# Kernel optimization log

Measured on AMD Instinct MI355X. Metric: run time of the kernel, lower is better.

Reference implementation:

```python
import jax, jax.numpy as jnp
import numpy as np

LAMBDA_TEMP = 20.0
GAMMA = 20.0
MARGIN = 0.05
EPS = 1e-8

B, K, M, D = 128, 256, 8, 128


def _unit(x, axis=-1):
    return x / jnp.linalg.norm(x, axis=axis, keepdims=True)


def setup_inputs() -> dict:
    key = jax.random.key(0)
    k1, k2, k3 = jax.random.split(key, 3)
    v_proj = _unit(jax.random.normal(k1, (B, K, D), dtype=jnp.float32))
    prototypes = _unit(jax.random.normal(k2, (K, M, D), dtype=jnp.float32))
    concept_labels = jax.random.randint(k3, (B, K), 0, 2, dtype=jnp.int64)
    return {"v_proj": v_proj, "concept_labels": concept_labels, "prototypes": prototypes}


def reference(v_proj, concept_labels, prototypes):
    # all-pairs prototype similarities: query vector (b,k) vs prototypes of concept c
    # sims: (B, K, C, M)
    sims = jnp.einsum('bkd,cmd->bkcm', v_proj, prototypes)
    # Eq.6: soft assignment over the M prototypes of each concept
    q = jax.nn.softmax(GAMMA * sims, axis=-1)
    # Eq.7-8: weighted similarity sim_c(v)  -> (B, K, C)
    sim = jnp.sum(q * sims, axis=-1)
    # positive similarity: concept k queried against its own prototypes, plus margin
    sim_pos = jnp.einsum('bkk->bk', sim) + MARGIN  # (B, K)
    # Eq.9: -log( exp(lam*sim_pos) / (sum_c exp(lam*sim_c) + eps) )
    denom = jnp.sum(jnp.exp(LAMBDA_TEMP * sim), axis=-1) + EPS  # (B, K)
    loss_bk = jnp.log(denom) - LAMBDA_TEMP * sim_pos  # (B, K)
    mask = (concept_labels == 1).astype(loss_bk.dtype)
    num_pos = jnp.sum(mask)
    total = jnp.sum(loss_bk * mask)
    return jnp.where(num_pos > 0, total / num_pos, total)
```

## Files before the change

### kernel.cpp

```cpp
#include <hip/hip_runtime.h>

#define NROWS 32768
#define LT 20.0f
#define CHUNKS 32

typedef _Float16 half8 __attribute__((ext_vector_type(8)));
typedef float    f32x4 __attribute__((ext_vector_type(4)));

__device__ __forceinline__ float swz16(float x) {
    return __int_as_float(__builtin_amdgcn_ds_swizzle(__float_as_int(x), 0x401F));
}

__global__ __launch_bounds__(1024)
void mpcl_main(const float* __restrict__ V,
               const int*   __restrict__ labels,
               const float* __restrict__ P,
               int* __restrict__ ws,
               float* __restrict__ out)
{
    __shared__ _Float16 Pst[2][64 * 128];
    __shared__ float sh_denom[128];
    __shared__ float sh_simpos[128];
    __shared__ float sh_red[32];

    int*   gcnt = ws;
    float* gsum = (float*)(ws + 2);

    const int tid  = threadIdx.x;
    const int lane = tid & 63;
    const int w    = tid >> 6;
    const int rg   = w >> 2;
    const int colq = w & 3;
    const int n    = lane & 15;
    const int q    = lane >> 4;
    const int rowbase = blockIdx.x * 128;
    const int cb   = colq * 16;

    if (tid < 128) { sh_denom[tid] = 0.0f; sh_simpos[tid] = 0.0f; }

    half8 vh[2][4];
#pragma unroll
    for (int rf = 0; rf < 2; ++rf) {
        const float* vr = V + (size_t)(rowbase + rg * 32 + rf * 16 + n) * 128 + q * 8;
#pragma unroll
        for (int c = 0; c < 4; ++c) {
            float4 x0 = *(const float4*)(vr + c * 32);
            float4 x1 = *(const float4*)(vr + c * 32 + 4);
            vh[rf][c][0] = (_Float16)x0.x; vh[rf][c][1] = (_Float16)x0.y;
            vh[rf][c][2] = (_Float16)x0.z; vh[rf][c][3] = (_Float16)x0.w;
            vh[rf][c][4] = (_Float16)x1.x; vh[rf][c][5] = (_Float16)x1.y;
            vh[rf][c][6] = (_Float16)x1.z; vh[rf][c][7] = (_Float16)x1.w;
        }
    }

    const int scol = tid >> 4;
    const int sdb  = tid & 15;
    const int sdbs = (sdb & 8) | ((sdb ^ scol) & 7);

    {
        const float* pp = P + (size_t)scol * 128 + sdb * 8;
        float4 a = *(const float4*)(pp);
        float4 b = *(const float4*)(pp + 4);
        half8 hv;
        hv[0] = (_Float16)a.x; hv[1] = (_Float16)a.y;
        hv[2] = (_Float16)a.z; hv[3] = (_Float16)a.w;
        hv[4] = (_Float16)b.x; hv[5] = (_Float16)b.y;
        hv[6] = (_Float16)b.z; hv[7] = (_Float16)b.w;
        *(half8*)&Pst[0][scol * 128 + sdbs * 8] = hv;
    }
    float4 pf0, pf1;
    {
        const float* pp = P + (size_t)(64 + scol) * 128 + sdb * 8;
        pf0 = *(const float4*)(pp);
        pf1 = *(const float4*)(pp + 4);
    }

    float dn[2] = {0.f, 0.f};

#pragma unroll 1
    for (int ch = 0; ch < CHUNKS; ++ch) {
        __syncthreads();

        half8 pf16[4];
#pragma unroll
        for (int c = 0; c < 4; ++c) {
            int dblk = c * 4 + q;
            int col  = cb + n;
            int dbs  = (dblk & 8) | ((dblk ^ col) & 7);
            pf16[c] = *(const half8*)&Pst[ch & 1][col * 128 + dbs * 8];
        }

        f32x4 acc[2] = {{0.f,0.f,0.f,0.f},{0.f,0.f,0.f,0.f}};
#pragma unroll
        for (int c = 0; c < 4; ++c)
#pragma unroll
            for (int rf = 0; rf < 2; ++rf)
                acc[rf] = __builtin_amdgcn_mfma_f32_16x16x32_f16(pf16[c], vh[rf][c], acc[rf], 0, 0, 0);

        if (ch < CHUNKS - 1) {
            half8 hv;
            hv[0] = (_Float16)pf0.x; hv[1] = (_Float16)pf0.y;
            hv[2] = (_Float16)pf0.z; hv[3] = (_Float16)pf0.w;
            hv[4] = (_Float16)pf1.x; hv[5] = (_Float16)pf1.y;
            hv[6] = (_Float16)pf1.z; hv[7] = (_Float16)pf1.w;
            *(half8*)&Pst[(ch + 1) & 1][scol * 128 + sdbs * 8] = hv;
        }
        if (ch < CHUNKS - 2) {
            const float* pp = P + (size_t)((ch + 2) * 64 + scol) * 128 + sdb * 8;
            pf0 = *(const float4*)(pp);
            pf1 = *(const float4*)(pp + 4);
        }

        const int cbase = ch * 8 + colq * 2;
        const int cA    = cbase + (q >> 1);
#pragma unroll
        for (int rf = 0; rf < 2; ++rf) {
            float s0 = acc[rf][0], s1 = acc[rf][1], s2 = acc[rf][2], s3 = acc[rf][3];
            float e0 = __expf(LT * s0), e1 = __expf(LT * s1);
            float e2 = __expf(LT * s2), e3 = __expf(LT * s3);
            float es = (e0 + e1) + (e2 + e3);
            float ss = fmaf(e0, s0, fmaf(e1, s1, fmaf(e2, s2, e3 * s3)));
            es += swz16(es);
            ss += swz16(ss);
            float simc = __fdividef(ss, es);
            dn[rf] += __expf(LT * simc);
            int rowloc = rg * 32 + rf * 16 + n;
            if (cA == ((rowbase + rowloc) & 255) && (q & 1) == 0)
                sh_simpos[rowloc] = simc;
        }
    }

#pragma unroll
    for (int rf = 0; rf < 2; ++rf) {
        float t = dn[rf];
        t += swz16(t);
        t += __shfl_xor(t, 32);
        if (q == 0)
            atomicAdd(&sh_denom[rg * 32 + rf * 16 + n], 0.5f * t);
    }
    __syncthreads();

    float s = 0.f, cc = 0.f;
    if (tid < 128) {
        int row = rowbase + tid;
        float lp = logf(sh_denom[tid] + 1e-8f) - LT * (sh_simpos[tid] + 0.05f);
        float mk = (labels[row] == 1) ? 1.0f : 0.0f;
        s = lp * mk;
        cc = mk;
    }
#pragma unroll
    for (int off = 32; off >= 1; off >>= 1) {
        s  += __shfl_down(s, off);
        cc += __shfl_down(cc, off);
    }
    if (lane == 0) { sh_red[w] = s; sh_red[16 + w] = cc; }
    __syncthreads();
    if (tid == 0) {
        s = 0.f; cc = 0.f;
#pragma unroll
        for (int i = 0; i < 16; ++i) { s += sh_red[i]; cc += sh_red[16 + i]; }
        atomicAdd(&gsum[0], s);
        atomicAdd(&gsum[1], cc);
        __threadfence();
        int g = __hip_atomic_fetch_add(gcnt, 1,
                                       __ATOMIC_ACQ_REL, __HIP_MEMORY_SCOPE_AGENT);
        if (g == 255) {
            __threadfence();
            float ts = __hip_atomic_load(&gsum[0], __ATOMIC_RELAXED, __HIP_MEMORY_SCOPE_AGENT);
            float tc = __hip_atomic_load(&gsum[1], __ATOMIC_RELAXED, __HIP_MEMORY_SCOPE_AGENT);
            out[0] = (tc > 0.0f) ? (ts / tc) : ts;
        }
    }
}

extern "C" void kernel_launch(void* const* d_in, const int* in_sizes, int n_in,
                              void* d_out, int out_size, void* d_ws, size_t ws_size,
                              hipStream_t stream)
{
    const float* V      = (const float*)d_in[0];
    const int*   labels = (const int*)d_in[1];
    const float* P      = (const float*)d_in[2];
    float* out = (float*)d_out;
    int*   ws  = (int*)d_ws;

    hipMemsetAsync(ws, 0, 16, stream);
    mpcl_main<<<256, 1024, 0, stream>>>(V, labels, P, ws, out);
}
```

Before: 115.5 us.

## Pre-convert prototypes to swizzled fp16 and stream via global_load_lds

Adds a prep kernel that converts the prototypes to fp16 once, in a pre-swizzled LDS layout. The main kernel then copies 128-column chunks directly into shared memory with global_load_lds, removing the per-block fp32 load, convert and LDS store work. Each wave now computes two MFMA tiles per chunk so that all 8 prototypes of a concept are held in one lane's registers. This removes the cross-lane swizzle reductions and halves the number of chunk iterations. The cost is an extra kernel launch and a workspace buffer.

```diff
diff --git a/kernel.cpp b/kernel.cpp
--- a/kernel.cpp
+++ b/kernel.cpp
@@ -2,23 +2,48 @@
 
 #define NROWS 32768
 #define LT 20.0f
-#define CHUNKS 32
+#define CHUNKS 16
 
 typedef _Float16 half8 __attribute__((ext_vector_type(8)));
 typedef float    f32x4 __attribute__((ext_vector_type(4)));
 
 __device__ __forceinline__ float swz16(float x) {
     return __int_as_float(__builtin_amdgcn_ds_swizzle(__float_as_int(x), 0x401F));
+}
+
+#define GLD16(gp, lp) __builtin_amdgcn_global_load_lds( \
+    (const __attribute__((address_space(1))) void*)(gp), \
+    (__attribute__((address_space(3))) void*)(lp), 16, 0, 0)
+
+__global__ __launch_bounds__(256)
+void mpcl_prep(const float* __restrict__ P, _Float16* __restrict__ Pw)
+{
+    int id   = blockIdx.x * 256 + threadIdx.x;
+    int gcol = id >> 4;
+    int dblk = id & 15;
+    int ch   = gcol >> 7;
+    int col  = gcol & 127;
+    int key  = (col & 3) | ((col & 8) >> 1);
+    int dbs  = (dblk & 8) | ((dblk ^ key) & 7);
+    const float* src = P + (size_t)gcol * 128 + dblk * 8;
+    float4 a = *(const float4*)src;
+    float4 b = *(const float4*)(src + 4);
+    half8 hv;
+    hv[0] = (_Float16)a.x; hv[1] = (_Float16)a.y;
+    hv[2] = (_Float16)a.z; hv[3] = (_Float16)a.w;
+    hv[4] = (_Float16)b.x; hv[5] = (_Float16)b.y;
+    hv[6] = (_Float16)b.z; hv[7] = (_Float16)b.w;
+    *(half8*)&Pw[((size_t)ch * 2048 + col * 16 + dbs) * 8] = hv;
 }
 
 __global__ __launch_bounds__(1024)
 void mpcl_main(const float* __restrict__ V,
                const int*   __restrict__ labels,
-               const float* __restrict__ P,
+               const _Float16* __restrict__ Pw,
                int* __restrict__ ws,
                float* __restrict__ out)
 {
-    __shared__ _Float16 Pst[2][64 * 128];
+    __shared__ __align__(16) _Float16 Pst[2][2048 * 8];
     __shared__ float sh_denom[128];
     __shared__ float sh_simpos[128];
     __shared__ float sh_red[32];
@@ -34,7 +59,6 @@
     const int n    = lane & 15;
     const int q    = lane >> 4;
     const int rowbase = blockIdx.x * 128;
-    const int cb   = colq * 16;
 
     if (tid < 128) { sh_denom[tid] = 0.0f; sh_simpos[tid] = 0.0f; }
 
@@ -53,27 +77,24 @@
         }
     }
 
-    const int scol = tid >> 4;
-    const int sdb  = tid & 15;
-    const int sdbs = (sdb & 8) | ((sdb ^ scol) & 7);
-
-    {
-        const float* pp = P + (size_t)scol * 128 + sdb * 8;
-        float4 a = *(const float4*)(pp);
-        float4 b = *(const float4*)(pp + 4);
-        half8 hv;
-        hv[0] = (_Float16)a.x; hv[1] = (_Float16)a.y;
-        hv[2] = (_Float16)a.z; hv[3] = (_Float16)a.w;
-        hv[4] = (_Float16)b.x; hv[5] = (_Float16)b.y;
-        hv[6] = (_Float16)b.z; hv[7] = (_Float16)b.w;
-        *(half8*)&Pst[0][scol * 128 + sdbs * 8] = hv;
-    }
-    float4 pf0, pf1;
-    {
-        const float* pp = P + (size_t)(64 + scol) * 128 + sdb * 8;
-        pf0 = *(const float4*)(pp);
-        pf1 = *(const float4*)(pp + 4);
-    }
+    const int col1 = colq * 32 + ((n >> 2) << 3) + (n & 3);
+    int off1[4];
+#pragma unroll
+    for (int c = 0; c < 4; ++c) {
+        int dblk = c * 4 + q;
+        int dbs  = (dblk & 8) | ((dblk ^ (n & 7)) & 7);
+        off1[c]  = (col1 * 16 + dbs) * 8;
+    }
+
+    const _Float16* gbase = Pw + (size_t)(w * 128 + lane) * 8;
+    _Float16* l0 = &Pst[0][(w * 128) * 8];
+    _Float16* l1 = &Pst[1][(w * 128) * 8];
+
+    GLD16(gbase,       l0);
+    GLD16(gbase + 512, l0 + 512);
+
+    const int rowk0 = (rowbase + rg * 32 + n) & 255;
+    const int rowk1 = (rowbase + rg * 32 + 16 + n) & 255;
 
     float dn[2] = {0.f, 0.f};
 
@@ -81,52 +102,43 @@
     for (int ch = 0; ch < CHUNKS; ++ch) {
         __syncthreads();
 
-        half8 pf16[4];
+        if (ch < CHUNKS - 1) {
+            const _Float16* g = gbase + (size_t)(ch + 1) * 16384;
+            _Float16* lnx = (ch & 1) ? l0 : l1;
+            GLD16(g,       lnx);
+            GLD16(g + 512, lnx + 512);
+        }
+
+        const _Float16* base = (ch & 1) ? &Pst[1][0] : &Pst[0][0];
+
+        f32x4 acc1[2] = {{0.f,0.f,0.f,0.f},{0.f,0.f,0.f,0.f}};
+        f32x4 acc2[2] = {{0.f,0.f,0.f,0.f},{0.f,0.f,0.f,0.f}};
 #pragma unroll
         for (int c = 0; c < 4; ++c) {
-            int dblk = c * 4 + q;
-            int col  = cb + n;
-            int dbs  = (dblk & 8) | ((dblk ^ col) & 7);
-            pf16[c] = *(const half8*)&Pst[ch & 1][col * 128 + dbs * 8];
-        }
-
-        f32x4 acc[2] = {{0.f,0.f,0.f,0.f},{0.f,0.f,0.f,0.f}};
-#pragma unroll
-        for (int c = 0; c < 4; ++c)
-#pragma unroll
-            for (int rf = 0; rf < 2; ++rf)
-                acc[rf] = __builtin_amdgcn_mfma_f32_16x16x32_f16(pf16[c], vh[rf][c], acc[rf], 0, 0, 0);
-
-        if (ch < CHUNKS - 1) {
-            half8 hv;
-            hv[0] = (_Float16)pf0.x; hv[1] = (_Float16)pf0.y;
-            hv[2] = (_Float16)pf0.z; hv[3] = (_Float16)pf0.w;
-            hv[4] = (_Float16)pf1.x; hv[5] = (_Float16)pf1.y;
-            hv[6] = (_Float16)pf1.z; hv[7] = (_Float16)pf1.w;
-            *(half8*)&Pst[(ch + 1) & 1][scol * 128 + sdbs * 8] = hv;
-        }
-        if (ch < CHUNKS - 2) {
-            const float* pp = P + (size_t)((ch + 2) * 64 + scol) * 128 + sdb * 8;
-            pf0 = *(const float4*)(pp);
-            pf1 = *(const float4*)(pp + 4);
-        }
-
-        const int cbase = ch * 8 + colq * 2;
-        const int cA    = cbase + (q >> 1);
+            half8 a1 = *(const half8*)&base[off1[c]];
+            half8 a2 = *(const half8*)&base[off1[c] + 512];
+            acc1[0] = __builtin_amdgcn_mfma_f32_16x16x32_f16(a1, vh[0][c], acc1[0], 0, 0, 0);
+            acc1[1] = __builtin_amdgcn_mfma_f32_16x16x32_f16(a1, vh[1][c], acc1[1], 0, 0, 0);
+            acc2[0] = __builtin_amdgcn_mfma_f32_16x16x32_f16(a2, vh[0][c], acc2[0], 0, 0, 0);
+            acc2[1] = __builtin_amdgcn_mfma_f32_16x16x32_f16(a2, vh[1][c], acc2[1], 0, 0, 0);
+        }
+
+        const int cA = ch * 16 + colq * 4 + q;
 #pragma unroll
         for (int rf = 0; rf < 2; ++rf) {
-            float s0 = acc[rf][0], s1 = acc[rf][1], s2 = acc[rf][2], s3 = acc[rf][3];
-            float e0 = __expf(LT * s0), e1 = __expf(LT * s1);
-            float e2 = __expf(LT * s2), e3 = __expf(LT * s3);
-            float es = (e0 + e1) + (e2 + e3);
-            float ss = fmaf(e0, s0, fmaf(e1, s1, fmaf(e2, s2, e3 * s3)));
-            es += swz16(es);
-            ss += swz16(ss);
+            float x0 = acc1[rf][0], x1 = acc1[rf][1], x2 = acc1[rf][2], x3 = acc1[rf][3];
+            float x4 = acc2[rf][0], x5 = acc2[rf][1], x6 = acc2[rf][2], x7 = acc2[rf][3];
+            float e0 = __expf(LT * x0), e1 = __expf(LT * x1);
+            float e2 = __expf(LT * x2), e3 = __expf(LT * x3);
+            float e4 = __expf(LT * x4), e5 = __expf(LT * x5);
+            float e6 = __expf(LT * x6), e7 = __expf(LT * x7);
+            float es = ((e0 + e1) + (e2 + e3)) + ((e4 + e5) + (e6 + e7));
+            float ss = fmaf(e0, x0, fmaf(e1, x1, fmaf(e2, x2, e3 * x3)))
+                     + fmaf(e4, x4, fmaf(e5, x5, fmaf(e6, x6, e7 * x7)));
             float simc = __fdividef(ss, es);
             dn[rf] += __expf(LT * simc);
-            int rowloc = rg * 32 + rf * 16 + n;
-            if (cA == ((rowbase + rowloc) & 255) && (q & 1) == 0)
-                sh_simpos[rowloc] = simc;
+            if (cA == (rf ? rowk1 : rowk0))
+                sh_simpos[rg * 32 + rf * 16 + n] = simc;
         }
     }
 
@@ -135,8 +147,8 @@
         float t = dn[rf];
         t += swz16(t);
         t += __shfl_xor(t, 32);
-        if (q == 0)
-            atomicAdd(&sh_denom[rg * 32 + rf * 16 + n], 0.5f * t);
+        if (lane < 16)
+            atomicAdd(&sh_denom[rg * 32 + rf * 16 + n], t);
     }
     __syncthreads();
 
@@ -182,7 +194,9 @@
     const float* P      = (const float*)d_in[2];
     float* out = (float*)d_out;
     int*   ws  = (int*)d_ws;
+    _Float16* Pw = (_Float16*)((char*)d_ws + 512);
 
     hipMemsetAsync(ws, 0, 16, stream);
-    mpcl_main<<<256, 1024, 0, stream>>>(V, labels, P, ws, out);
-}
+    mpcl_prep<<<128, 256, 0, stream>>>(P, Pw);
+    mpcl_main<<<256, 1024, 0, stream>>>(V, labels, Pw, ws, out);
+}
```

Measured after the change: 110.4 us. 1.05x faster.
